# Optimization experiments

Measured on AMD Instinct MI355X. Metric: run time of the kernel, lower is better.

## Reference

```python
import jax, jax.numpy as jnp
import numpy as np


def setup_inputs() -> dict:
    key = jax.random.key(0)
    k1, k2 = jax.random.split(key)
    B, N, M, D = 8, 8192, 8192, 3
    gts = jax.random.normal(k1, (B, N, D), dtype=jnp.float32)
    preds = jax.random.normal(k2, (B, M, D), dtype=jnp.float32)
    return {"gts": gts, "preds": preds}


def reference(gts, preds):
    # Chamfer distance (pytorch3d defaults): squared L2, mean over points,
    # mean over batch, sum of both directions.
    x2 = jnp.sum(gts * gts, axis=-1)          # [B, N]
    y2 = jnp.sum(preds * preds, axis=-1)      # [B, M]
    xy = jnp.einsum('bnd,bmd->bnm', gts, preds)  # [B, N, M]
    d2 = x2[:, :, None] + y2[:, None, :] - 2.0 * xy
    d2 = jnp.maximum(d2, 0.0)  # guard tiny negative values from cancellation
    cham_x = jnp.mean(jnp.min(d2, axis=2))  # x -> nearest y, mean over N then B
    cham_y = jnp.mean(jnp.min(d2, axis=1))  # y -> nearest x, mean over M then B
    return cham_x + cham_y
```

## Files before the change

kernel.cpp:

```cpp
#include <hip/hip_runtime.h>
#include <hip/hip_bf16.h>
#include <math.h>


#define BLOCK 256
#define WAVES 4
#define QPW 64
#define NCHUNK 2
#define SREF 512
#define STAGE_BYTES (SREF * 32)
#define IPS (SREF / 64)

typedef short short8 __attribute__((ext_vector_type(8)));
typedef float f32x16 __attribute__((ext_vector_type(16)));
typedef unsigned int u32;
typedef __attribute__((address_space(1))) const u32 gu32;
typedef __attribute__((address_space(3))) u32 lu32;

__device__ __forceinline__ unsigned int bf16hi(float f) {
    __hip_bfloat16 h = __float2bfloat16(f);
    return (unsigned int)*reinterpret_cast<unsigned short*>(&h);
}
__device__ __forceinline__ float bf16f(unsigned int u) {
    unsigned short us = (unsigned short)u;
    __hip_bfloat16 h;
    *reinterpret_cast<unsigned short*>(&h) = us;
    return __bfloat162float(h);
}

#define MFMA(a, b, c) __builtin_amdgcn_mfma_f32_32x32x16_bf16((a), (b), (c), 0, 0, 0)

__device__ __forceinline__ void gload_lds16(const void* g, void* l) {
    __builtin_amdgcn_global_load_lds((gu32*)g, (lu32*)l, 16, 0, 0);
}

__global__ void prep_kernel(const float* __restrict__ gts, const float* __restrict__ preds,
                            int nG, int nP, uint4* __restrict__ recQ,
                            unsigned char* __restrict__ recB, float* __restrict__ q2,
                            float* out) {
    const int idx = blockIdx.x * blockDim.x + threadIdx.x;
    if (idx == 0) out[0] = 0.0f;
    if (idx >= nG + nP) return;
    const float* src;
    unsigned char* rb;
    if (idx < nG) {
        src = gts + 3 * (size_t)idx;
        rb  = recB + (size_t)(idx >> 5) * 1024 + (size_t)(idx & 31) * 16;
    } else {
        const int j = idx - nG;
        src = preds + 3 * (size_t)j;
        rb  = recB + (size_t)nG * 32 + (size_t)(j >> 5) * 1024 + (size_t)(j & 31) * 16;
    }
    const float x = src[0], y = src[1], z = src[2];
    const float n2 = x * x + y * y + z * z;
    const float w = -0.5f * n2;
    q2[idx] = n2;
    const unsigned int xh = bf16hi(x), yh = bf16hi(y), zh = bf16hi(z), wh = bf16hi(w);
    const unsigned int xl = bf16hi(x - bf16f(xh));
    const unsigned int yl = bf16hi(y - bf16f(yh));
    const unsigned int zl = bf16hi(z - bf16f(zh));
    const unsigned int wl = bf16hi(w - bf16f(wh));
    const unsigned int hx = xh | (yh << 16), hz = zh | (wh << 16);
    const unsigned int lx = xl | (yl << 16), lz = zl | (wl << 16);
    recQ[idx] = make_uint4(hx, hz, lx, lz);
    *(uint4*)(rb)       = make_uint4(hx, hz, hx, hz);
    *(uint4*)(rb + 512) = make_uint4(lx, lz, 0u, 0u);
}

__global__ void __launch_bounds__(BLOCK, 2)
nn_kernel(const uint4* __restrict__ recQ, const unsigned char* __restrict__ recB,
          float* __restrict__ kpart, int N, int M, int B) {
    const int z = blockIdx.z;
    const bool dirX = (z < B);
    const int b = dirX ? z : z - B;
    const int NQ = dirX ? N : M;
    const int NR = dirX ? M : N;
    const uint4* Qr = recQ + (dirX ? 0 : (size_t)B * N) + (size_t)b * NQ;
    const int chunk = NR / NCHUNK;
    const unsigned char* Rb = recB + (dirX ? (size_t)B * N * 32 : 0)
                              + ((size_t)b * NR + (size_t)blockIdx.y * chunk) * 32;
    const int nGP = B * (N + M);
    float* outK = kpart + (size_t)blockIdx.y * nGP + (dirX ? 0 : B * N) + (size_t)b * NQ;

    const int tid = threadIdx.x;
    const int lane = tid & 63;
    const int wave = tid >> 6;
    const int m = lane & 31;
    const unsigned int loMask = (lane >= 32) ? 0u : 0xFFFFFFFFu;
    const int qBase = (blockIdx.x * WAVES + wave) * QPW;

    const uint4 q0 = Qr[qBase + m];
    const uint4 q1 = Qr[qBase + 32 + m];
    union { uint4 v; short8 s; } a;
    a.v.x = q0.x;
    a.v.y = (q0.y & 0xFFFFu) | 0x3F800000u;
    a.v.z = q0.z & loMask;
    a.v.w = q0.w & 0xFFFFu & loMask;
    const short8 A0 = a.s;
    a.v.x = q1.x;
    a.v.y = (q1.y & 0xFFFFu) | 0x3F800000u;
    a.v.z = q1.z & loMask;
    a.v.w = q1.w & 0xFFFFu & loMask;
    const short8 A1 = a.s;

    f32x16 k0, k1, zc;
    #pragma unroll
    for (int r = 0; r < 16; ++r) { k0[r] = -INFINITY; k1[r] = -INFINITY; zc[r] = 0.0f; }

    __shared__ __align__(16) unsigned char smem[WAVES * 64 * 36 * 4];

    const unsigned char* gsrc = Rb + (size_t)wave * 4096 + (size_t)lane * 16;
    unsigned char* lbase = smem + wave * 4096;
    auto stage_issue = [&](int s) {
        const unsigned char* g = gsrc + (size_t)s * STAGE_BYTES;
        unsigned char* l = lbase + ((s & 1) * STAGE_BYTES);
        #pragma unroll
        for (int k2 = 0; k2 < 4; ++k2)
            gload_lds16(g + k2 * 1024, l + k2 * 1024);
    };

    const int nStages = chunk / SREF;
    stage_issue(0);
    __syncthreads();

    #pragma unroll 1
    for (int s = 0; s < nStages; ++s) {
        if (s + 1 < nStages) stage_issue(s + 1);
        const unsigned char* tb = smem + ((s & 1) * STAGE_BYTES) + lane * 16;
        #pragma unroll
        for (int i = 0; i < IPS; ++i) {
            const short8 b0 = *(const short8*)(tb + i * 2048);
            const short8 b1 = *(const short8*)(tb + i * 2048 + 1024);
            const f32x16 c0 = MFMA(A0, b0, zc);
            const f32x16 c1 = MFMA(A0, b1, zc);
            const f32x16 c2 = MFMA(A1, b0, zc);
            const f32x16 c3 = MFMA(A1, b1, zc);
            #pragma unroll
            for (int r = 0; r < 16; ++r)
                k0[r] = fmaxf(fmaxf(c0[r], c1[r]), k0[r]);
            #pragma unroll
            for (int r = 0; r < 16; ++r)
                k1[r] = fmaxf(fmaxf(c2[r], c3[r]), k1[r]);
        }
        __syncthreads();
    }

    float (*sT)[64][36] = (float (*)[64][36])smem;
    #pragma unroll
    for (int r = 0; r < 16; ++r) {
        const int row = (r & 3) + 8 * (r >> 2) + 4 * (lane >> 5);
        sT[wave][row][m]      = k0[r];
        sT[wave][32 + row][m] = k1[r];
    }
    const float4* rowp = (const float4*)&sT[wave][lane][0];
    float4 m01 = rowp[0];
    #pragma unroll
    for (int kk = 1; kk < 8; ++kk) {
        const float4 t = rowp[kk];
        m01.x = fmaxf(m01.x, t.x); m01.y = fmaxf(m01.y, t.y);
        m01.z = fmaxf(m01.z, t.z); m01.w = fmaxf(m01.w, t.w);
    }
    const float cmax = fmaxf(fmaxf(m01.x, m01.y), fmaxf(m01.z, m01.w));
    outK[qBase + lane] = cmax;
}

__global__ void __launch_bounds__(BLOCK)
reduce_kernel(const float* __restrict__ kpart, const float* __restrict__ q2,
              int nG, int nP, float invx, float invy, float* __restrict__ out) {
    const int total = nG + nP;
    float local = 0.0f;
    for (int idx = blockIdx.x * blockDim.x + threadIdx.x; idx < total;
         idx += gridDim.x * blockDim.x) {
        const float c = fmaxf(kpart[idx], kpart[total + idx]);
        const float inv = (idx < nG) ? invx : invy;
        local += fmaxf(q2[idx] - 2.0f * c, 0.0f) * inv;
    }
    __shared__ float waveSums[BLOCK / 64];
    float v = local;
    #pragma unroll
    for (int off = 32; off; off >>= 1) v += __shfl_xor(v, off);
    if ((threadIdx.x & 63) == 0) waveSums[threadIdx.x >> 6] = v;
    __syncthreads();
    if (threadIdx.x == 0) {
        float s = 0.0f;
        #pragma unroll
        for (int w = 0; w < BLOCK / 64; ++w) s += waveSums[w];
        atomicAdd(out, s);
    }
}

extern "C" void kernel_launch(void* const* d_in, const int* in_sizes, int n_in,
                              void* d_out, int out_size, void* d_ws, size_t ws_size,
                              hipStream_t stream) {
    const float* gts   = (const float*)d_in[0];
    const float* preds = (const float*)d_in[1];
    float* out = (float*)d_out;

    const int B = 8;
    const int N = in_sizes[0] / (B * 3);
    const int M = in_sizes[1] / (B * 3);
    const int nG = B * N, nP = B * M;

    uint4* recQ = (uint4*)d_ws;
    unsigned char* recB = (unsigned char*)(recQ + nG + nP);
    float* kpart = (float*)(recB + (size_t)(nG + nP) * 32);
    float* q2    = kpart + (size_t)NCHUNK * (nG + nP);

    prep_kernel<<<(nG + nP + BLOCK - 1) / BLOCK, BLOCK, 0, stream>>>(
        gts, preds, nG, nP, recQ, recB, q2, out);

    dim3 grid(N / (WAVES * QPW), NCHUNK, 2 * B);
    nn_kernel<<<grid, BLOCK, 0, stream>>>(recQ, recB, kpart, N, M, B);

    reduce_kernel<<<256, BLOCK, 0, stream>>>(
        kpart, q2, nG, nP, 1.0f / (float)nG, 1.0f / (float)nP, out);
}
```

Baseline: 98.12 us.

## Load reference tiles directly into registers with double buffering instead of LDS staging

New measurement: 99.98 us. No clear change (+1.9%).

```diff
diff --git a/kernel.cpp b/kernel.cpp
--- a/kernel.cpp
+++ b/kernel.cpp
@@ -7,15 +7,9 @@
 #define WAVES 4
 #define QPW 64
 #define NCHUNK 2
-#define SREF 512
-#define STAGE_BYTES (SREF * 32)
-#define IPS (SREF / 64)
 
 typedef short short8 __attribute__((ext_vector_type(8)));
 typedef float f32x16 __attribute__((ext_vector_type(16)));
-typedef unsigned int u32;
-typedef __attribute__((address_space(1))) const u32 gu32;
-typedef __attribute__((address_space(3))) u32 lu32;
 
 __device__ __forceinline__ unsigned int bf16hi(float f) {
     __hip_bfloat16 h = __float2bfloat16(f);
@@ -30,9 +24,7 @@
 
 #define MFMA(a, b, c) __builtin_amdgcn_mfma_f32_32x32x16_bf16((a), (b), (c), 0, 0, 0)
 
-__device__ __forceinline__ void gload_lds16(const void* g, void* l) {
-    __builtin_amdgcn_global_load_lds((gu32*)g, (lu32*)l, 16, 0, 0);
-}
+union U4S { uint4 v; short8 s; };
 
 __global__ void prep_kernel(const float* __restrict__ gts, const float* __restrict__ preds,
                             int nG, int nP, uint4* __restrict__ recQ,
@@ -68,7 +60,7 @@
 }
 
 __global__ void __launch_bounds__(BLOCK, 2)
-nn_kernel(const uint4* __restrict__ recQ, const unsigned char* __restrict__ recB,
+nn_kernel(const uint4* __restrict__ recQ, const uint4* __restrict__ recB,
           float* __restrict__ kpart, int N, int M, int B) {
     const int z = blockIdx.z;
     const bool dirX = (z < B);
@@ -77,8 +69,8 @@
     const int NR = dirX ? M : N;
     const uint4* Qr = recQ + (dirX ? 0 : (size_t)B * N) + (size_t)b * NQ;
     const int chunk = NR / NCHUNK;
-    const unsigned char* Rb = recB + (dirX ? (size_t)B * N * 32 : 0)
-                              + ((size_t)b * NR + (size_t)blockIdx.y * chunk) * 32;
+    const uint4* Rb4 = recB + (dirX ? (size_t)B * N * 2 : 0)
+                       + ((size_t)b * NR + (size_t)blockIdx.y * chunk) * 2;
     const int nGP = B * (N + M);
     float* outK = kpart + (size_t)blockIdx.y * nGP + (dirX ? 0 : B * N) + (size_t)b * NQ;
 
@@ -107,45 +99,48 @@
     #pragma unroll
     for (int r = 0; r < 16; ++r) { k0[r] = -INFINITY; k1[r] = -INFINITY; zc[r] = 0.0f; }
 
-    __shared__ __align__(16) unsigned char smem[WAVES * 64 * 36 * 4];
-
-    const unsigned char* gsrc = Rb + (size_t)wave * 4096 + (size_t)lane * 16;
-    unsigned char* lbase = smem + wave * 4096;
-    auto stage_issue = [&](int s) {
-        const unsigned char* g = gsrc + (size_t)s * STAGE_BYTES;
-        unsigned char* l = lbase + ((s & 1) * STAGE_BYTES);
-        #pragma unroll
-        for (int k2 = 0; k2 < 4; ++k2)
-            gload_lds16(g + k2 * 1024, l + k2 * 1024);
-    };
-
-    const int nStages = chunk / SREF;
-    stage_issue(0);
-    __syncthreads();
-
+    const int rot = ((wave + blockIdx.x) & 3) << 5;
+
+#define LOADG(P, g) do {                                                     \
+        const uint4* p_ = Rb4 + (size_t)((((g) * 8 + rot) & 127) * 64) + lane; \
+        P##0 = p_[0];   P##1 = p_[64];  P##2 = p_[128]; P##3 = p_[192];      \
+        P##4 = p_[256]; P##5 = p_[320]; P##6 = p_[384]; P##7 = p_[448];      \
+    } while (0)
+
+#define DO2(ba, bb) do {                                                     \
+        U4S ua_, ub_; ua_.v = (ba); ub_.v = (bb);                            \
+        const f32x16 c0_ = MFMA(A0, ua_.s, zc);                              \
+        const f32x16 c1_ = MFMA(A0, ub_.s, zc);                              \
+        const f32x16 c2_ = MFMA(A1, ua_.s, zc);                              \
+        const f32x16 c3_ = MFMA(A1, ub_.s, zc);                              \
+        _Pragma("unroll")                                                    \
+        for (int r = 0; r < 16; ++r)                                         \
+            k0[r] = fmaxf(fmaxf(c0_[r], c1_[r]), k0[r]);                     \
+        _Pragma("unroll")                                                    \
+        for (int r = 0; r < 16; ++r)                                         \
+            k1[r] = fmaxf(fmaxf(c2_[r], c3_[r]), k1[r]);                     \
+    } while (0)
+
+#define COMPG(P) do {                                                        \
+        DO2(P##0, P##1); DO2(P##2, P##3);                                    \
+        DO2(P##4, P##5); DO2(P##6, P##7);                                    \
+    } while (0)
+
+    uint4 S0, S1, S2, S3, S4, S5, S6, S7;
+    uint4 T0, T1, T2, T3, T4, T5, T6, T7;
+    LOADG(S, 0);
     #pragma unroll 1
-    for (int s = 0; s < nStages; ++s) {
-        if (s + 1 < nStages) stage_issue(s + 1);
-        const unsigned char* tb = smem + ((s & 1) * STAGE_BYTES) + lane * 16;
-        #pragma unroll
-        for (int i = 0; i < IPS; ++i) {
-            const short8 b0 = *(const short8*)(tb + i * 2048);
-            const short8 b1 = *(const short8*)(tb + i * 2048 + 1024);
-            const f32x16 c0 = MFMA(A0, b0, zc);
-            const f32x16 c1 = MFMA(A0, b1, zc);
-            const f32x16 c2 = MFMA(A1, b0, zc);
-            const f32x16 c3 = MFMA(A1, b1, zc);
-            #pragma unroll
-            for (int r = 0; r < 16; ++r)
-                k0[r] = fmaxf(fmaxf(c0[r], c1[r]), k0[r]);
-            #pragma unroll
-            for (int r = 0; r < 16; ++r)
-                k1[r] = fmaxf(fmaxf(c2[r], c3[r]), k1[r]);
-        }
-        __syncthreads();
-    }
-
-    float (*sT)[64][36] = (float (*)[64][36])smem;
+    for (int g = 0; g < 16; g += 2) {
+        LOADG(T, g + 1);
+        COMPG(S);
+        LOADG(S, g + 2);
+        COMPG(T);
+    }
+#undef LOADG
+#undef DO2
+#undef COMPG
+
+    __shared__ float sT[WAVES][64][36];
     #pragma unroll
     for (int r = 0; r < 16; ++r) {
         const int row = (r & 3) + 8 * (r >> 2) + 4 * (lane >> 5);
@@ -210,7 +205,7 @@
         gts, preds, nG, nP, recQ, recB, q2, out);
 
     dim3 grid(N / (WAVES * QPW), NCHUNK, 2 * B);
-    nn_kernel<<<grid, BLOCK, 0, stream>>>(recQ, recB, kpart, N, M, B);
+    nn_kernel<<<grid, BLOCK, 0, stream>>>(recQ, (const uint4*)recB, kpart, N, M, B);
 
     reduce_kernel<<<256, BLOCK, 0, stream>>>(
         kpart, q2, nG, nP, 1.0f / (float)nG, 1.0f / (float)nP, out);
```
